# Performance work log

Hardware: AMD Instinct MI355X
Metric: run time of the kernel (lower is better)

The kernel has to match this reference:

```python
import jax, jax.numpy as jnp
import numpy as np
import math

SLEEP_DIM = 1024
BRAIN_DIM = 512
N_HEADS = 8
D_K = SLEEP_DIM // N_HEADS
N_S = 2048
N_C = 4096
LN_EPS = 1e-5


def setup_inputs() -> dict:
    key = jax.random.key(0)
    ks = jax.random.split(key, 9)
    s = 0.02  # weight init scale
    return {
        "H_S": jax.random.normal(ks[0], (N_S, SLEEP_DIM), dtype=jnp.float32),
        "H_C": jax.random.normal(ks[1], (N_C, BRAIN_DIM), dtype=jnp.float32),
        "G_glyph": jax.random.uniform(ks[2], (N_S, N_C), dtype=jnp.float32),
        "W_Q": jax.random.normal(ks[3], (SLEEP_DIM, SLEEP_DIM), dtype=jnp.float32) * s,
        "W_K": jax.random.normal(ks[4], (SLEEP_DIM, BRAIN_DIM), dtype=jnp.float32) * s,
        "W_V": jax.random.normal(ks[5], (SLEEP_DIM, BRAIN_DIM), dtype=jnp.float32) * s,
        "W_O": jax.random.normal(ks[6], (SLEEP_DIM, SLEEP_DIM), dtype=jnp.float32) * s,
        "b_O": jnp.zeros((SLEEP_DIM,), dtype=jnp.float32),
        "ln_gamma": jnp.ones((SLEEP_DIM,), dtype=jnp.float32),
        "ln_beta": jnp.zeros((SLEEP_DIM,), dtype=jnp.float32),
    }


def reference(H_S, H_C, G_glyph, W_Q, W_K, W_V, W_O, b_O, ln_gamma, ln_beta):
    # projections (torch Linear: x @ W.T)
    Q = (H_S @ W_Q.T).reshape(N_S, N_HEADS, D_K)   # (N_S, H, d_k)
    K = (H_C @ W_K.T).reshape(N_C, N_HEADS, D_K)   # (N_C, H, d_k)
    V = (H_C @ W_V.T).reshape(N_C, N_HEADS, D_K)   # (N_C, H, d_k)

    # scores: (N_S, N_C, H), scaled then multiplicatively gated per (s, c) pair
    scores = jnp.einsum("shd,chd->sch", Q, K) / math.sqrt(D_K)
    scores = scores * G_glyph[:, :, None]

    # softmax over keys (dim=1 of (N_S, N_C, H)); dropout is identity at eval
    attn = jax.nn.softmax(scores, axis=1)

    # weighted value sum, merge heads
    H_new = jnp.einsum("sch,chd->shd", attn, V).reshape(N_S, SLEEP_DIM)
    H_new = H_new @ W_O.T + b_O

    # residual + LayerNorm
    x = H_new + H_S
    mu = jnp.mean(x, axis=-1, keepdims=True)
    var = jnp.var(x, axis=-1, keepdims=True)
    out = (x - mu) / jnp.sqrt(var + LN_EPS) * ln_gamma + ln_beta
    return out, attn.mean(-1)
```

## Files before the change

kernel.cpp:

```cpp
#include <hip/hip_runtime.h>
#include <hip/hip_bf16.h>

#define NS 2048
#define NC 4096
#define SD 1024
#define BD 512
#define NH 8
#define DK 128

typedef __bf16 bf16;
typedef __bf16 bf16x8 __attribute__((ext_vector_type(8)));
typedef __bf16 bf16x4 __attribute__((ext_vector_type(4)));
typedef float f32x4 __attribute__((ext_vector_type(4)));

__device__ __forceinline__ bf16 f2bf(float f) { return (bf16)f; }
__device__ __forceinline__ bf16x8 ld8(const bf16* p) { return *(const bf16x8*)p; }
__device__ __forceinline__ f32x4 mfma16(bf16x8 a, bf16x8 b, f32x4 c) {
  return __builtin_amdgcn_mfma_f32_16x16x32_bf16(a, b, c, 0, 0, 0);
}

__global__ void k_cast(const float* __restrict__ in, bf16* __restrict__ out, int n4) {
  int i = blockIdx.x * blockDim.x + threadIdx.x;
  int stride = gridDim.x * blockDim.x;
  for (; i < n4; i += stride) {
    float4 v = ((const float4*)in)[i];
    bf16x4 o;
    o[0] = f2bf(v.x); o[1] = f2bf(v.y); o[2] = f2bf(v.z); o[3] = f2bf(v.w);
    ((bf16x4*)out)[i] = o;
  }
}

template <typename CT>
__global__ __launch_bounds__(256) void k_gemm_bt(const bf16* __restrict__ A,
                                                 const bf16* __restrict__ B,
                                                 CT* __restrict__ C,
                                                 int M, int N, int K) {
  __shared__ bf16 As[128 * 64];
  __shared__ bf16 Bs[64 * 64];
  const int tid = threadIdx.x;
  const int l = tid & 63, w = tid >> 6;
  const int g = l >> 4, r15 = l & 15;
  const int m0 = blockIdx.y * 128, n0 = blockIdx.x * 64;
  const int wm = (w >> 1) * 64, wn = (w & 1) * 32;
  f32x4 acc[4][2] = {};
  for (int k0 = 0; k0 < K; k0 += 64) {
    __syncthreads();
#pragma unroll
    for (int i = 0; i < 4; i++) {
      int slot = tid + i * 256;
      int row = slot >> 3, cp = slot & 7;
      int gc = cp ^ (row & 7);
      *(uint4*)(As + slot * 8) = *(const uint4*)(A + (size_t)(m0 + row) * K + k0 + gc * 8);
    }
#pragma unroll
    for (int i = 0; i < 2; i++) {
      int slot = tid + i * 256;
      int row = slot >> 3, cp = slot & 7;
      int gc = cp ^ (row & 7);
      *(uint4*)(Bs + slot * 8) = *(const uint4*)(B + (size_t)(n0 + row) * K + k0 + gc * 8);
    }
    __syncthreads();
#pragma unroll
    for (int kk = 0; kk < 2; kk++) {
      bf16x8 af[4], bfr[2];
#pragma unroll
      for (int mi = 0; mi < 4; mi++) {
        int row = wm + mi * 16 + r15;
        int cidx = (kk * 4 + g) ^ (row & 7);
        af[mi] = *(const bf16x8*)(As + row * 64 + cidx * 8);
      }
#pragma unroll
      for (int ni = 0; ni < 2; ni++) {
        int row = wn + ni * 16 + r15;
        int cidx = (kk * 4 + g) ^ (row & 7);
        bfr[ni] = *(const bf16x8*)(Bs + row * 64 + cidx * 8);
      }
#pragma unroll
      for (int mi = 0; mi < 4; mi++)
#pragma unroll
        for (int ni = 0; ni < 2; ni++)
          acc[mi][ni] = mfma16(af[mi], bfr[ni], acc[mi][ni]);
    }
  }
#pragma unroll
  for (int mi = 0; mi < 4; mi++)
#pragma unroll
    for (int ni = 0; ni < 2; ni++)
#pragma unroll
      for (int rr = 0; rr < 4; rr++) {
        int mrow = m0 + wm + mi * 16 + g * 4 + rr;
        int ncol = n0 + wn + ni * 16 + r15;
        float v = acc[mi][ni][rr];
        if constexpr (sizeof(CT) == 4) C[(size_t)mrow * N + ncol] = v;
        else                           C[(size_t)mrow * N + ncol] = f2bf(v);
      }
}

__global__ __launch_bounds__(256) void k_transpose(const bf16* __restrict__ V, bf16* __restrict__ Vt) {
  __shared__ bf16 tile[32][33];
  const int t = threadIdx.x;
  const int col = t & 31, r0 = t >> 5;
  const int cbase = blockIdx.y * 32;
  const int dbase = blockIdx.x * 32;
#pragma unroll
  for (int i = 0; i < 4; i++) {
    int r = r0 + i * 8;
    tile[r][col] = V[(size_t)(cbase + r) * SD + dbase + col];
  }
  __syncthreads();
#pragma unroll
  for (int i = 0; i < 4; i++) {
    int r = r0 + i * 8;
    Vt[(size_t)(dbase + r) * NC + cbase + col] = tile[col][r];
  }
}

__global__ __launch_bounds__(256) void k_attn(const bf16* __restrict__ Q, const bf16* __restrict__ Km,
                                              const bf16* __restrict__ Vt, const float* __restrict__ Gf,
                                              float* __restrict__ inv_l, bf16* __restrict__ Hattn) {
  __shared__ bf16 p_lds[4][512];
  __shared__ float O_red[4][16][128];
  __shared__ float red[4][16];
  __shared__ float invl_s[16];
  const int tid = threadIdx.x;
  const int l = tid & 63, w = tid >> 6;
  const int g = l >> 4, r15 = l & 15;
  const int row_l = g * 4;
  const int s0 = blockIdx.x * 16;
  const int h = blockIdx.y;
  const int hoff = h * DK;
  const float scale = 0.08838834764831845f;
  bf16* pw = &p_lds[w][0];

  bf16x8 qf[4];
#pragma unroll
  for (int kk = 0; kk < 4; kk++)
    qf[kk] = ld8(Q + (size_t)(s0 + r15) * SD + hoff + kk * 32 + g * 8);

  float psum[4] = {0.f, 0.f, 0.f, 0.f};
  f32x4 oacc[8] = {};
  const int cbeg = w * 1024, cend = cbeg + 1024;
  for (int c0 = cbeg; c0 < cend; c0 += 32) {
#pragma unroll
    for (int sub = 0; sub < 2; sub++) {
      const int cb = c0 + sub * 16;
      f32x4 acc = {0.f, 0.f, 0.f, 0.f};
#pragma unroll
      for (int kk = 0; kk < 4; kk++)
        acc = mfma16(qf[kk], ld8(Km + (size_t)(cb + r15) * SD + hoff + kk * 32 + g * 8), acc);
#pragma unroll
      for (int rr = 0; rr < 4; rr++) {
        const int prow = row_l + rr;
        float gv = Gf[(size_t)(s0 + prow) * NC + cb + r15];
        float p = __expf(acc[rr] * scale * gv);
        psum[rr] += p;
        int off = (prow * 64 + (sub * 16 + r15) * 2) ^ (((prow >> 1) & 3) << 4);
        *(bf16*)((char*)pw + off) = f2bf(p);
      }
    }
    const int offr = r15 * 64 + ((g ^ ((r15 >> 1) & 3)) << 4);
    bf16x8 pf = *(const bf16x8*)((const char*)pw + offr);
#pragma unroll
    for (int nf = 0; nf < 8; nf++) {
      bf16x8 vf = ld8(Vt + (size_t)(hoff + nf * 16 + r15) * NC + c0 + g * 8);
      oacc[nf] = mfma16(pf, vf, oacc[nf]);
    }
  }
#pragma unroll
  for (int rr = 0; rr < 4; rr++) {
    float v = psum[rr];
    v += __shfl_xor(v, 1); v += __shfl_xor(v, 2);
    v += __shfl_xor(v, 4); v += __shfl_xor(v, 8);
    psum[rr] = v;
  }
  if (r15 == 0) {
#pragma unroll
    for (int rr = 0; rr < 4; rr++) red[w][row_l + rr] = psum[rr];
  }
  __syncthreads();
  if (tid < 16) {
    float tot = red[0][tid] + red[1][tid] + red[2][tid] + red[3][tid];
    float iv = 1.0f / tot;
    invl_s[tid] = iv;
    inv_l[(size_t)(s0 + tid) * NH + h] = iv;
  }
  __syncthreads();
  float il[4];
#pragma unroll
  for (int rr = 0; rr < 4; rr++) il[rr] = invl_s[row_l + rr];
#pragma unroll
  for (int nf = 0; nf < 8; nf++)
#pragma unroll
    for (int rr = 0; rr < 4; rr++)
      O_red[w][row_l + rr][nf * 16 + r15] = oacc[nf][rr] * il[rr];
  __syncthreads();
  {
    const int row = tid >> 4, d0 = (tid & 15) * 8;
    bf16 pk[8] __attribute__((aligned(16)));
#pragma unroll
    for (int j = 0; j < 8; j++) {
      float s = O_red[0][row][d0 + j] + O_red[1][row][d0 + j] +
                O_red[2][row][d0 + j] + O_red[3][row][d0 + j];
      pk[j] = f2bf(s);
    }
    *(uint4*)(Hattn + (size_t)(s0 + row) * SD + hoff + d0) = *(const uint4*)pk;
  }
}

__global__ __launch_bounds__(256) void k_attn_mean(const bf16* __restrict__ Q, const bf16* __restrict__ Km,
                                                   const float* __restrict__ Gf, const float* __restrict__ inv_l,
                                                   float* __restrict__ out_mean) {
  __shared__ bf16 Qs[16 * 1024];
  const int tid = threadIdx.x;
  const int l = tid & 63, w = tid >> 6;
  const int g = l >> 4, r15 = l & 15;
  const int row_l = g * 4;
  const int s0 = blockIdx.y * 16;
  const int c0 = blockIdx.x * 64 + w * 16;
  const float scale = 0.08838834764831845f;
#pragma unroll
  for (int i = 0; i < 8; i++) {
    int slot = tid + i * 256;
    int row = slot >> 7, cp = slot & 127;
    int gc = cp ^ (row & 7);
    *(uint4*)(Qs + slot * 8) = *(const uint4*)(Q + (size_t)(s0 + row) * SD + gc * 8);
  }
  __syncthreads();
  float gv[4];
#pragma unroll
  for (int rr = 0; rr < 4; rr++)
    gv[rr] = Gf[(size_t)(s0 + row_l + rr) * NC + c0 + r15];
  float macc[4] = {0.f, 0.f, 0.f, 0.f};
  for (int h = 0; h < NH; h++) {
    bf16x8 qf[4];
#pragma unroll
    for (int kk = 0; kk < 4; kk++) {
      int cidx = h * 16 + kk * 4 + g;
      int slot = cidx ^ (r15 & 7);
      qf[kk] = *(const bf16x8*)(Qs + r15 * 1024 + slot * 8);
    }
    f32x4 acc = {0.f, 0.f, 0.f, 0.f};
#pragma unroll
    for (int kk = 0; kk < 4; kk++)
      acc = mfma16(qf[kk], ld8(Km + (size_t)(c0 + r15) * SD + h * DK + kk * 32 + g * 8), acc);
#pragma unroll
    for (int rr = 0; rr < 4; rr++) {
      float iv = inv_l[(size_t)(s0 + row_l + rr) * NH + h];
      macc[rr] += __expf(acc[rr] * scale * gv[rr]) * iv;
    }
  }
#pragma unroll
  for (int rr = 0; rr < 4; rr++)
    out_mean[(size_t)(s0 + row_l + rr) * NC + c0 + r15] = macc[rr] * 0.125f;
}

__global__ __launch_bounds__(256) void k_ln(const float* __restrict__ Op, const float* __restrict__ HS,
                                            const float* __restrict__ bO, const float* __restrict__ gamma,
                                            const float* __restrict__ beta, float* __restrict__ out) {
  __shared__ float rs[4][2];
  const int row = blockIdx.x, t = threadIdx.x;
  const int l = t & 63, w = t >> 6;
  float4 xo = *(const float4*)(Op + (size_t)row * SD + t * 4);
  float4 hs = *(const float4*)(HS + (size_t)row * SD + t * 4);
  float4 bo = *(const float4*)(bO + t * 4);
  float x[4] = {xo.x + hs.x + bo.x, xo.y + hs.y + bo.y,
                xo.z + hs.z + bo.z, xo.w + hs.w + bo.w};
  float s = x[0] + x[1] + x[2] + x[3];
  float q = x[0] * x[0] + x[1] * x[1] + x[2] * x[2] + x[3] * x[3];
#pragma unroll
  for (int m = 1; m < 64; m <<= 1) { s += __shfl_xor(s, m); q += __shfl_xor(q, m); }
  if (l == 0) { rs[w][0] = s; rs[w][1] = q; }
  __syncthreads();
  s = rs[0][0] + rs[1][0] + rs[2][0] + rs[3][0];
  q = rs[0][1] + rs[1][1] + rs[2][1] + rs[3][1];
  float mean = s * (1.0f / SD);
  float var = q * (1.0f / SD) - mean * mean;
  float rstd = rsqrtf(var + 1e-5f);
  float4 gm = *(const float4*)(gamma + t * 4);
  float4 bt = *(const float4*)(beta + t * 4);
  float4 o;
  o.x = (x[0] - mean) * rstd * gm.x + bt.x;
  o.y = (x[1] - mean) * rstd * gm.y + bt.y;
  o.z = (x[2] - mean) * rstd * gm.z + bt.z;
  o.w = (x[3] - mean) * rstd * gm.w + bt.w;
  *(float4*)(out + (size_t)row * SD + t * 4) = o;
}

extern "C" void kernel_launch(void* const* d_in, const int* in_sizes, int n_in,
                              void* d_out, int out_size, void* d_ws, size_t ws_size,
                              hipStream_t stream) {
  const float* H_S = (const float*)d_in[0];
  const float* H_C = (const float*)d_in[1];
  const float* G   = (const float*)d_in[2];
  const float* W_Q = (const float*)d_in[3];
  const float* W_K = (const float*)d_in[4];
  const float* W_V = (const float*)d_in[5];
  const float* W_O = (const float*)d_in[6];
  const float* b_O = (const float*)d_in[7];
  const float* gam = (const float*)d_in[8];
  const float* bet = (const float*)d_in[9];
  float* out = (float*)d_out;
  float* out_mean = out + (size_t)NS * SD;

  char* p = (char*)d_ws;
  auto alloc = [&](size_t bytes) { char* r = p; p += (bytes + 255) & ~(size_t)255; return r; };
  bf16* HSb = (bf16*)alloc((size_t)NS * SD * 2);
  bf16* HCb = (bf16*)alloc((size_t)NC * BD * 2);
  bf16* WQb = (bf16*)alloc((size_t)SD * SD * 2);
  bf16* WKb = (bf16*)alloc((size_t)SD * BD * 2);
  bf16* WVb = (bf16*)alloc((size_t)SD * BD * 2);
  bf16* WOb = (bf16*)alloc((size_t)SD * SD * 2);
  bf16* Qb  = (bf16*)alloc((size_t)NS * SD * 2);
  bf16* Kb  = (bf16*)alloc((size_t)NC * SD * 2);
  bf16* Vb  = (bf16*)alloc((size_t)NC * SD * 2);
  bf16* Vtb = (bf16*)alloc((size_t)SD * NC * 2);
  bf16* Hat = (bf16*)alloc((size_t)NS * SD * 2);
  float* Opj  = (float*)alloc((size_t)NS * SD * 4);
  float* invl = (float*)alloc((size_t)NS * NH * 4);

  k_cast<<<1024, 256, 0, stream>>>(H_S, HSb, NS * SD / 4);
  k_cast<<<1024, 256, 0, stream>>>(H_C, HCb, NC * BD / 4);
  k_cast<<<1024, 256, 0, stream>>>(W_Q, WQb, SD * SD / 4);
  k_cast<<<1024, 256, 0, stream>>>(W_K, WKb, SD * BD / 4);
  k_cast<<<1024, 256, 0, stream>>>(W_V, WVb, SD * BD / 4);
  k_cast<<<1024, 256, 0, stream>>>(W_O, WOb, SD * SD / 4);

  k_gemm_bt<bf16><<<dim3(SD / 64, NS / 128), 256, 0, stream>>>(HSb, WQb, Qb, NS, SD, SD);
  k_gemm_bt<bf16><<<dim3(SD / 64, NC / 128), 256, 0, stream>>>(HCb, WKb, Kb, NC, SD, BD);
  k_gemm_bt<bf16><<<dim3(SD / 64, NC / 128), 256, 0, stream>>>(HCb, WVb, Vb, NC, SD, BD);
  k_transpose<<<dim3(SD / 32, NC / 32), 256, 0, stream>>>(Vb, Vtb);
  k_attn<<<dim3(NS / 16, NH), 256, 0, stream>>>(Qb, Kb, Vtb, G, invl, Hat);
  k_attn_mean<<<dim3(NC / 64, NS / 16), 256, 0, stream>>>(Qb, Kb, G, invl, out_mean);
  k_gemm_bt<float><<<dim3(SD / 64, NS / 128), 256, 0, stream>>>(Hat, WOb, Opj, NS, SD, SD);
  k_ln<<<NS, 256, 0, stream>>>(Opj, H_S, b_O, gam, bet, out);
}
```

Baseline: 590.6 us.

## Tile attention with LDS-staged K/V, split keys across blocks, add combine pass

Rewrites the attention kernel so each block handles 128 query rows for one head and a quarter of the keys. K and V tiles are staged through swizzled LDS with register prefetch, so each tile is reused across four waves instead of every wave reading it from global memory. Partial outputs and softmax sums go to a workspace that aliases the cast buffers, and a new combine kernel reduces them. The attention-mean kernel is also re-tiled to 64x64 blocks that share staged Q/K, at the cost of an extra launch and partial-output traffic.

```diff
diff --git a/kernel.cpp b/kernel.cpp
--- a/kernel.cpp
+++ b/kernel.cpp
@@ -115,143 +115,243 @@
   }
 }
 
-__global__ __launch_bounds__(256) void k_attn(const bf16* __restrict__ Q, const bf16* __restrict__ Km,
-                                              const bf16* __restrict__ Vt, const float* __restrict__ Gf,
-                                              float* __restrict__ inv_l, bf16* __restrict__ Hattn) {
-  __shared__ bf16 p_lds[4][512];
-  __shared__ float O_red[4][16][128];
-  __shared__ float red[4][16];
-  __shared__ float invl_s[16];
+__global__ __launch_bounds__(256) void k_attn2(const bf16* __restrict__ Q, const bf16* __restrict__ Km,
+                                               const bf16* __restrict__ Vt, const float* __restrict__ Gf,
+                                               float* __restrict__ psum_part, bf16* __restrict__ Opart) {
+  __shared__ bf16 Kl[64 * 128];
+  __shared__ bf16 Vl[128 * 64];
+  __shared__ bf16 Pl[4][32 * 64];
   const int tid = threadIdx.x;
   const int l = tid & 63, w = tid >> 6;
   const int g = l >> 4, r15 = l & 15;
-  const int row_l = g * 4;
-  const int s0 = blockIdx.x * 16;
-  const int h = blockIdx.y;
-  const int hoff = h * DK;
+  const int s0 = blockIdx.x * 128;
+  const int h = blockIdx.y, hoff = h * DK;
+  const int ch = blockIdx.z;
+  const int cbase = ch * (NC / 4);
   const float scale = 0.08838834764831845f;
-  bf16* pw = &p_lds[w][0];
-
-  bf16x8 qf[4];
-#pragma unroll
-  for (int kk = 0; kk < 4; kk++)
-    qf[kk] = ld8(Q + (size_t)(s0 + r15) * SD + hoff + kk * 32 + g * 8);
-
-  float psum[4] = {0.f, 0.f, 0.f, 0.f};
-  f32x4 oacc[8] = {};
-  const int cbeg = w * 1024, cend = cbeg + 1024;
-  for (int c0 = cbeg; c0 < cend; c0 += 32) {
-#pragma unroll
-    for (int sub = 0; sub < 2; sub++) {
-      const int cb = c0 + sub * 16;
-      f32x4 acc = {0.f, 0.f, 0.f, 0.f};
+  char* KlB = (char*)Kl;
+  char* VlB = (char*)Vl;
+  char* PlB = (char*)Pl[w];
+  const int swz = r15 & 7;
+
+  bf16x8 qf[2][4];
+#pragma unroll
+  for (int smi = 0; smi < 2; smi++)
+#pragma unroll
+    for (int kk = 0; kk < 4; kk++)
+      qf[smi][kk] = ld8(Q + (size_t)(s0 + w * 32 + smi * 16 + r15) * SD + hoff + kk * 32 + g * 8);
+
+  f32x4 oacc[8][2] = {};
+  float psum[2] = {0.f, 0.f};
+
+  const int krow0 = tid >> 4, ksl = tid & 15;
+  const int vrow0 = tid >> 3, vsl = tid & 7;
+
+  uint4 kreg[4], vreg[4];
+  auto loadstep = [&](int cb) {
+#pragma unroll
+    for (int i = 0; i < 4; i++)
+      kreg[i] = *(const uint4*)(Km + (size_t)(cb + krow0 + i * 16) * SD + hoff + ksl * 8);
+#pragma unroll
+    for (int i = 0; i < 4; i++)
+      vreg[i] = *(const uint4*)(Vt + (size_t)(hoff + vrow0 + i * 32) * NC + cb + vsl * 8);
+  };
+  loadstep(cbase);
+
+  for (int t = 0; t < 16; ++t) {
+    const int cb = cbase + t * 64;
+    __syncthreads();
+#pragma unroll
+    for (int i = 0; i < 4; i++) {
+      int row = krow0 + i * 16;
+      *(uint4*)(KlB + row * 256 + ((ksl ^ (row & 7)) << 4)) = kreg[i];
+    }
+#pragma unroll
+    for (int i = 0; i < 4; i++) {
+      int row = vrow0 + i * 32;
+      *(uint4*)(VlB + row * 128 + ((vsl ^ (row & 7)) << 4)) = vreg[i];
+    }
+    __syncthreads();
+    if (t < 15) loadstep(cb + 64);
+#pragma unroll
+    for (int csub = 0; csub < 4; ++csub) {
+      bf16x8 kf[4];
 #pragma unroll
       for (int kk = 0; kk < 4; kk++)
-        acc = mfma16(qf[kk], ld8(Km + (size_t)(cb + r15) * SD + hoff + kk * 32 + g * 8), acc);
-#pragma unroll
-      for (int rr = 0; rr < 4; rr++) {
-        const int prow = row_l + rr;
-        float gv = Gf[(size_t)(s0 + prow) * NC + cb + r15];
-        float p = __expf(acc[rr] * scale * gv);
-        psum[rr] += p;
-        int off = (prow * 64 + (sub * 16 + r15) * 2) ^ (((prow >> 1) & 3) << 4);
-        *(bf16*)((char*)pw + off) = f2bf(p);
-      }
-    }
-    const int offr = r15 * 64 + ((g ^ ((r15 >> 1) & 3)) << 4);
-    bf16x8 pf = *(const bf16x8*)((const char*)pw + offr);
-#pragma unroll
-    for (int nf = 0; nf < 8; nf++) {
-      bf16x8 vf = ld8(Vt + (size_t)(hoff + nf * 16 + r15) * NC + c0 + g * 8);
-      oacc[nf] = mfma16(pf, vf, oacc[nf]);
-    }
-  }
-#pragma unroll
-  for (int rr = 0; rr < 4; rr++) {
-    float v = psum[rr];
-    v += __shfl_xor(v, 1); v += __shfl_xor(v, 2);
-    v += __shfl_xor(v, 4); v += __shfl_xor(v, 8);
-    psum[rr] = v;
-  }
-  if (r15 == 0) {
-#pragma unroll
-    for (int rr = 0; rr < 4; rr++) red[w][row_l + rr] = psum[rr];
+        kf[kk] = *(const bf16x8*)(KlB + (csub * 16 + r15) * 256 + (((kk * 4 + g) ^ swz) << 4));
+#pragma unroll
+      for (int smi = 0; smi < 2; smi++) {
+        f32x4 a = {0.f, 0.f, 0.f, 0.f};
+#pragma unroll
+        for (int kk = 0; kk < 4; kk++) a = mfma16(kf[kk], qf[smi][kk], a);
+        const int srow = s0 + w * 32 + smi * 16 + r15;
+        float4 gv = *(const float4*)(Gf + (size_t)srow * NC + cb + csub * 16 + g * 4);
+        float p0 = __expf(a[0] * scale * gv.x);
+        float p1 = __expf(a[1] * scale * gv.y);
+        float p2 = __expf(a[2] * scale * gv.z);
+        float p3 = __expf(a[3] * scale * gv.w);
+        psum[smi] += (p0 + p1) + (p2 + p3);
+        bf16 pk[4] __attribute__((aligned(8)));
+        pk[0] = f2bf(p0); pk[1] = f2bf(p1); pk[2] = f2bf(p2); pk[3] = f2bf(p3);
+        *(uint2*)(PlB + (smi * 16 + r15) * 128 + ((csub * 32 + g * 8) ^ (swz << 4))) = *(const uint2*)pk;
+      }
+    }
+#pragma unroll
+    for (int kc = 0; kc < 2; ++kc) {
+      bf16x8 pf[2];
+#pragma unroll
+      for (int smi = 0; smi < 2; smi++)
+        pf[smi] = *(const bf16x8*)(PlB + (smi * 16 + r15) * 128 + ((kc * 64 + g * 16) ^ (swz << 4)));
+#pragma unroll
+      for (int nf = 0; nf < 8; ++nf) {
+        bf16x8 vf = *(const bf16x8*)(VlB + (nf * 16 + r15) * 128 + (((kc * 4 + g) ^ swz) << 4));
+#pragma unroll
+        for (int smi = 0; smi < 2; smi++)
+          oacc[nf][smi] = mfma16(vf, pf[smi], oacc[nf][smi]);
+      }
+    }
+  }
+#pragma unroll
+  for (int smi = 0; smi < 2; smi++) {
+    float ps = psum[smi];
+    ps += __shfl_xor(ps, 16);
+    ps += __shfl_xor(ps, 32);
+    if (g == 0) {
+      int srow = s0 + w * 32 + smi * 16 + r15;
+      psum_part[((size_t)ch * NS + srow) * NH + h] = ps;
+    }
+  }
+#pragma unroll
+  for (int nf = 0; nf < 8; nf++)
+#pragma unroll
+    for (int smi = 0; smi < 2; smi++) {
+      int srow = s0 + w * 32 + smi * 16 + r15;
+      bf16 ob[4] __attribute__((aligned(8)));
+#pragma unroll
+      for (int rr = 0; rr < 4; rr++) ob[rr] = f2bf(oacc[nf][smi][rr]);
+      *(uint2*)(Opart + ((size_t)ch * NS + srow) * SD + hoff + nf * 16 + g * 4) = *(const uint2*)ob;
+    }
+}
+
+__global__ __launch_bounds__(256) void k_combine(const float* __restrict__ psum_part,
+                                                 const bf16* __restrict__ Opart,
+                                                 bf16* __restrict__ Hat, float* __restrict__ inv_l) {
+  __shared__ float il_s[NH];
+  const int row = blockIdx.x, t = threadIdx.x;
+  if (t < NH) {
+    float s = 0.f;
+#pragma unroll
+    for (int ch = 0; ch < 4; ch++) s += psum_part[((size_t)ch * NS + row) * NH + t];
+    float iv = 1.0f / s;
+    il_s[t] = iv;
+    inv_l[(size_t)row * NH + t] = iv;
   }
   __syncthreads();
-  if (tid < 16) {
-    float tot = red[0][tid] + red[1][tid] + red[2][tid] + red[3][tid];
-    float iv = 1.0f / tot;
-    invl_s[tid] = iv;
-    inv_l[(size_t)(s0 + tid) * NH + h] = iv;
-  }
-  __syncthreads();
-  float il[4];
-#pragma unroll
-  for (int rr = 0; rr < 4; rr++) il[rr] = invl_s[row_l + rr];
-#pragma unroll
-  for (int nf = 0; nf < 8; nf++)
-#pragma unroll
-    for (int rr = 0; rr < 4; rr++)
-      O_red[w][row_l + rr][nf * 16 + r15] = oacc[nf][rr] * il[rr];
-  __syncthreads();
-  {
-    const int row = tid >> 4, d0 = (tid & 15) * 8;
-    bf16 pk[8] __attribute__((aligned(16)));
-#pragma unroll
-    for (int j = 0; j < 8; j++) {
-      float s = O_red[0][row][d0 + j] + O_red[1][row][d0 + j] +
-                O_red[2][row][d0 + j] + O_red[3][row][d0 + j];
-      pk[j] = f2bf(s);
-    }
-    *(uint4*)(Hattn + (size_t)(s0 + row) * SD + hoff + d0) = *(const uint4*)pk;
-  }
-}
-
-__global__ __launch_bounds__(256) void k_attn_mean(const bf16* __restrict__ Q, const bf16* __restrict__ Km,
-                                                   const float* __restrict__ Gf, const float* __restrict__ inv_l,
-                                                   float* __restrict__ out_mean) {
-  __shared__ bf16 Qs[16 * 1024];
+  const int d0 = t * 4;
+  float acc[4] = {0.f, 0.f, 0.f, 0.f};
+#pragma unroll
+  for (int ch = 0; ch < 4; ch++) {
+    bf16x4 v = *(const bf16x4*)(Opart + ((size_t)ch * NS + row) * SD + d0);
+#pragma unroll
+    for (int j = 0; j < 4; j++) acc[j] += (float)v[j];
+  }
+  float iv = il_s[d0 >> 7];
+  bf16 ob[4] __attribute__((aligned(8)));
+#pragma unroll
+  for (int j = 0; j < 4; j++) ob[j] = f2bf(acc[j] * iv);
+  *(uint2*)(Hat + (size_t)row * SD + d0) = *(const uint2*)ob;
+}
+
+__global__ __launch_bounds__(256) void k_mean2(const bf16* __restrict__ Q, const bf16* __restrict__ Km,
+                                               const float* __restrict__ Gf, const float* __restrict__ inv_l,
+                                               float* __restrict__ out_mean) {
+  __shared__ bf16 Klm[64 * 128];
+  __shared__ bf16 Qlm[64 * 128];
   const int tid = threadIdx.x;
   const int l = tid & 63, w = tid >> 6;
   const int g = l >> 4, r15 = l & 15;
-  const int row_l = g * 4;
-  const int s0 = blockIdx.y * 16;
-  const int c0 = blockIdx.x * 64 + w * 16;
+  const int ws = w >> 1, wc = w & 1;
+  const int c0 = blockIdx.x * 64, s0 = blockIdx.y * 64;
   const float scale = 0.08838834764831845f;
-#pragma unroll
-  for (int i = 0; i < 8; i++) {
-    int slot = tid + i * 256;
-    int row = slot >> 7, cp = slot & 127;
-    int gc = cp ^ (row & 7);
-    *(uint4*)(Qs + slot * 8) = *(const uint4*)(Q + (size_t)(s0 + row) * SD + gc * 8);
-  }
-  __syncthreads();
-  float gv[4];
-#pragma unroll
-  for (int rr = 0; rr < 4; rr++)
-    gv[rr] = Gf[(size_t)(s0 + row_l + rr) * NC + c0 + r15];
-  float macc[4] = {0.f, 0.f, 0.f, 0.f};
-  for (int h = 0; h < NH; h++) {
-    bf16x8 qf[4];
-#pragma unroll
-    for (int kk = 0; kk < 4; kk++) {
-      int cidx = h * 16 + kk * 4 + g;
-      int slot = cidx ^ (r15 & 7);
-      qf[kk] = *(const bf16x8*)(Qs + r15 * 1024 + slot * 8);
-    }
-    f32x4 acc = {0.f, 0.f, 0.f, 0.f};
-#pragma unroll
-    for (int kk = 0; kk < 4; kk++)
-      acc = mfma16(qf[kk], ld8(Km + (size_t)(c0 + r15) * SD + h * DK + kk * 32 + g * 8), acc);
-#pragma unroll
-    for (int rr = 0; rr < 4; rr++) {
-      float iv = inv_l[(size_t)(s0 + row_l + rr) * NH + h];
-      macc[rr] += __expf(acc[rr] * scale * gv[rr]) * iv;
-    }
-  }
-#pragma unroll
-  for (int rr = 0; rr < 4; rr++)
-    out_mean[(size_t)(s0 + row_l + rr) * NC + c0 + r15] = macc[rr] * 0.125f;
+  const int swz = r15 & 7;
+  char* KB = (char*)Klm;
+  char* QB = (char*)Qlm;
+  const int row0 = tid >> 4, sl = tid & 15;
+
+  float4 gv[2][2];
+#pragma unroll
+  for (int smi = 0; smi < 2; smi++)
+#pragma unroll
+    for (int csub = 0; csub < 2; csub++)
+      gv[smi][csub] = *(const float4*)(Gf + (size_t)(s0 + ws * 32 + smi * 16 + r15) * NC +
+                                       c0 + wc * 32 + csub * 16 + g * 4);
+
+  f32x4 macc[2][2] = {};
+  uint4 kreg[4], qreg[4];
+  auto loadh = [&](int h) {
+#pragma unroll
+    for (int i = 0; i < 4; i++)
+      kreg[i] = *(const uint4*)(Km + (size_t)(c0 + row0 + i * 16) * SD + h * DK + sl * 8);
+#pragma unroll
+    for (int i = 0; i < 4; i++)
+      qreg[i] = *(const uint4*)(Q + (size_t)(s0 + row0 + i * 16) * SD + h * DK + sl * 8);
+  };
+  loadh(0);
+  for (int h = 0; h < NH; ++h) {
+    __syncthreads();
+#pragma unroll
+    for (int i = 0; i < 4; i++) {
+      int row = row0 + i * 16;
+      *(uint4*)(KB + row * 256 + ((sl ^ (row & 7)) << 4)) = kreg[i];
+    }
+#pragma unroll
+    for (int i = 0; i < 4; i++) {
+      int row = row0 + i * 16;
+      *(uint4*)(QB + row * 256 + ((sl ^ (row & 7)) << 4)) = qreg[i];
+    }
+    __syncthreads();
+    if (h < NH - 1) loadh(h + 1);
+    bf16x8 kf[2][4], qfr[2][4];
+#pragma unroll
+    for (int csub = 0; csub < 2; csub++)
+#pragma unroll
+      for (int kk = 0; kk < 4; kk++)
+        kf[csub][kk] = *(const bf16x8*)(KB + (wc * 32 + csub * 16 + r15) * 256 + (((kk * 4 + g) ^ swz) << 4));
+#pragma unroll
+    for (int smi = 0; smi < 2; smi++)
+#pragma unroll
+      for (int kk = 0; kk < 4; kk++)
+        qfr[smi][kk] = *(const bf16x8*)(QB + (ws * 32 + smi * 16 + r15) * 256 + (((kk * 4 + g) ^ swz) << 4));
+    float ilv[2];
+#pragma unroll
+    for (int smi = 0; smi < 2; smi++)
+      ilv[smi] = inv_l[(size_t)(s0 + ws * 32 + smi * 16 + r15) * NH + h];
+#pragma unroll
+    for (int smi = 0; smi < 2; smi++)
+#pragma unroll
+      for (int csub = 0; csub < 2; csub++) {
+        f32x4 a = {0.f, 0.f, 0.f, 0.f};
+#pragma unroll
+        for (int kk = 0; kk < 4; kk++) a = mfma16(kf[csub][kk], qfr[smi][kk], a);
+        float4 gvv = gv[smi][csub];
+        macc[smi][csub][0] += __expf(a[0] * scale * gvv.x) * ilv[smi];
+        macc[smi][csub][1] += __expf(a[1] * scale * gvv.y) * ilv[smi];
+        macc[smi][csub][2] += __expf(a[2] * scale * gvv.z) * ilv[smi];
+        macc[smi][csub][3] += __expf(a[3] * scale * gvv.w) * ilv[smi];
+      }
+  }
+#pragma unroll
+  for (int smi = 0; smi < 2; smi++)
+#pragma unroll
+    for (int csub = 0; csub < 2; csub++) {
+      int srow = s0 + ws * 32 + smi * 16 + r15;
+      float4 o;
+      o.x = macc[smi][csub][0] * 0.125f;
+      o.y = macc[smi][csub][1] * 0.125f;
+      o.z = macc[smi][csub][2] * 0.125f;
+      o.w = macc[smi][csub][3] * 0.125f;
+      *(float4*)(out_mean + (size_t)srow * NC + c0 + wc * 32 + csub * 16 + g * 4) = o;
+    }
 }
 
 __global__ __launch_bounds__(256) void k_ln(const float* __restrict__ Op, const float* __restrict__ HS,
@@ -304,19 +404,22 @@
 
   char* p = (char*)d_ws;
   auto alloc = [&](size_t bytes) { char* r = p; p += (bytes + 255) & ~(size_t)255; return r; };
-  bf16* HSb = (bf16*)alloc((size_t)NS * SD * 2);
-  bf16* HCb = (bf16*)alloc((size_t)NC * BD * 2);
-  bf16* WQb = (bf16*)alloc((size_t)SD * SD * 2);
-  bf16* WKb = (bf16*)alloc((size_t)SD * BD * 2);
-  bf16* WVb = (bf16*)alloc((size_t)SD * BD * 2);
+  char* region0 = alloc((size_t)20 << 20);
+  bf16* HSb = (bf16*)region0;
+  bf16* HCb = (bf16*)(region0 + ((size_t)4 << 20));
+  bf16* WQb = (bf16*)(region0 + ((size_t)8 << 20));
+  bf16* WKb = (bf16*)(region0 + ((size_t)10 << 20));
+  bf16* WVb = (bf16*)(region0 + ((size_t)11 << 20));
+  bf16* Vb  = (bf16*)(region0 + ((size_t)12 << 20));
+  bf16* Opart = (bf16*)region0;
   bf16* WOb = (bf16*)alloc((size_t)SD * SD * 2);
   bf16* Qb  = (bf16*)alloc((size_t)NS * SD * 2);
   bf16* Kb  = (bf16*)alloc((size_t)NC * SD * 2);
-  bf16* Vb  = (bf16*)alloc((size_t)NC * SD * 2);
   bf16* Vtb = (bf16*)alloc((size_t)SD * NC * 2);
   bf16* Hat = (bf16*)alloc((size_t)NS * SD * 2);
-  float* Opj  = (float*)alloc((size_t)NS * SD * 4);
+  float* Opj = (float*)alloc((size_t)NS * SD * 4);
   float* invl = (float*)alloc((size_t)NS * NH * 4);
+  float* psum_part = (float*)alloc((size_t)4 * NS * NH * 4);
 
   k_cast<<<1024, 256, 0, stream>>>(H_S, HSb, NS * SD / 4);
   k_cast<<<1024, 256, 0, stream>>>(H_C, HCb, NC * BD / 4);
@@ -329,8 +432,11 @@
   k_gemm_bt<bf16><<<dim3(SD / 64, NC / 128), 256, 0, stream>>>(HCb, WKb, Kb, NC, SD, BD);
   k_gemm_bt<bf16><<<dim3(SD / 64, NC / 128), 256, 0, stream>>>(HCb, WVb, Vb, NC, SD, BD);
   k_transpose<<<dim3(SD / 32, NC / 32), 256, 0, stream>>>(Vb, Vtb);
-  k_attn<<<dim3(NS / 16, NH), 256, 0, stream>>>(Qb, Kb, Vtb, G, invl, Hat);
-  k_attn_mean<<<dim3(NC / 64, NS / 16), 256, 0, stream>>>(Qb, Kb, G, invl, out_mean);
+
+  k_attn2<<<dim3(NS / 128, NH, 4), 256, 0, stream>>>(Qb, Kb, Vtb, G, psum_part, Opart);
+  k_combine<<<NS, 256, 0, stream>>>(psum_part, Opart, Hat, invl);
+  k_mean2<<<dim3(NC / 64, NS / 64), 256, 0, stream>>>(Qb, Kb, G, invl, out_mean);
+
   k_gemm_bt<float><<<dim3(SD / 64, NS / 128), 256, 0, stream>>>(Hat, WOb, Opj, NS, SD, SD);
   k_ln<<<NS, 256, 0, stream>>>(Opj, H_S, b_O, gam, bet, out);
 }
```

New measurement: 516.0 us. 12.6% less time.
